# Performance work log

Hardware: AMD Instinct MI355X
Metric: run time of the kernel (lower is better)

Reference implementation:

```python
import jax, jax.numpy as jnp
import numpy as np

EPS = 1e-6
INV_T = 1.0
STEPS = 6  # TRAIN_STEPS (module defaults to training mode)
NORM_EPS = 1e-12  # F.normalize default eps


def _l2norm_dim1(t):
    # F.normalize(t, p=2, dim=1): divide by clamped L2 norm over feature dim D
    n = jnp.sqrt(jnp.sum(t * t, axis=1, keepdims=True))
    return t / jnp.maximum(n, NORM_EPS)


def setup_inputs() -> dict:
    key = jax.random.key(0)
    k1, k2 = jax.random.split(key)
    x5d = jax.random.normal(k1, (2, 512, 16, 64, 64), dtype=jnp.float32)
    bases = jax.random.uniform(k2, (2, 512, 64), dtype=jnp.float32)  # (B*S, D_feat, R)
    return {"x5d": x5d, "bases": bases}


def reference(x5d, bases):
    B, C, Dv, H, W = x5d.shape
    S = 1
    D_feat = C // S
    N = Dv * H * W
    x = x5d.reshape(B * S, D_feat, N)  # (BS, D, N)

    b = _l2norm_dim1(bases)  # _build_bases normalizes over D
    # coef init uses UNCLAMPED x (clamp happens in-place only inside local_step)
    coef = jax.nn.softmax(INV_T * jnp.einsum('bdn,bdr->bnr', x, b), axis=-1)

    xc = jnp.maximum(x, EPS)  # clamp_input_nonneg, applied in-place on first MU step

    def mu_step(carry, _):
        b, c = carry
        BtB = jnp.einsum('bdr,bds->brs', b, b)            # (BS,R,R)
        numC = jnp.einsum('bdn,bdr->bnr', xc, b)          # (BS,N,R)
        denC = jnp.einsum('bnr,brs->bns', c, BtB) + EPS
        c = c * numC / denC
        CtC = jnp.einsum('bnr,bns->brs', c, c)            # (BS,R,R)
        numB = jnp.einsum('bdn,bnr->bdr', xc, c)          # (BS,D,R)
        denB = jnp.einsum('bdr,brs->bds', b, CtC) + EPS
        b = b * numB / denB
        b = jnp.maximum(b, EPS)
        c = jnp.maximum(c, EPS)
        b = _l2norm_dim1(b)  # normalize_each_step
        return (b, c), None

    (b, coef), _ = jax.lax.scan(mu_step, (b, coef), None, length=STEPS)

    # compute_coef (differentiable refinement in the original)
    BtB = jnp.einsum('bdr,bds->brs', b, b)
    numC = jnp.einsum('bdn,bdr->bnr', xc, b)
    denC = jnp.einsum('bnr,brs->bns', coef, BtB) + EPS
    c_new = coef * (numC / denC)

    x_hat = jnp.einsum('bdr,bnr->bdn', b, c_new)  # (BS, D, N)
    return x_hat.reshape(B, C, Dv, H, W)
```

## Files before the change

kernel.cpp:

```cpp
#include <hip/hip_runtime.h>
#include <math.h>

#define DD   512
#define NTOT 65536
#define RR   64
#define NB   2
#define EPSV 1e-6f

typedef unsigned short u16;
typedef __attribute__((ext_vector_type(8))) short bf16x8;
typedef __attribute__((ext_vector_type(8))) unsigned short us8;
typedef __attribute__((ext_vector_type(4))) unsigned short us4;
typedef __attribute__((ext_vector_type(4))) float f32x4;

__device__ inline u16 f2bf(float f) {
    union { float f; unsigned u; } x; x.f = f;
    unsigned r = x.u + 0x7FFFu + ((x.u >> 16) & 1u);
    return (u16)(r >> 16);
}
__device__ inline float bf2f(u16 h) {
    union { unsigned u; float f; } x; x.u = ((unsigned)h) << 16;
    return x.f;
}
__device__ inline bf16x8 clampbf8(bf16x8 v) {
#pragma unroll
    for (int i = 0; i < 8; ++i) {
        short t = v[i];
        v[i] = (t < (short)0x3586) ? (short)0x3586 : t;
    }
    return v;
}

#define MFMA16(a, b, c) __builtin_amdgcn_mfma_f32_16x16x32_bf16((a), (b), (c), 0, 0, 0)

__global__ __launch_bounds__(256) void convert_x_kernel(const float* __restrict__ x,
                                                        u16* __restrict__ xd,
                                                        u16* __restrict__ xT) {
    int s = blockIdx.z, d0 = blockIdx.y * 64, n0 = blockIdx.x * 64;
    const float* xp = x + ((size_t)s * DD + d0) * NTOT + n0;
    u16* xdp = xd + ((size_t)s * DD + d0) * NTOT + n0;
    u16* xtp = xT + ((size_t)s * NTOT + n0) * DD + d0;
    __shared__ u16 L[64][66];
    int tid = threadIdx.x;
#pragma unroll
    for (int k = 0; k < 4; ++k) {
        int f4 = tid + k * 256;
        int dr = f4 >> 4, c4 = (f4 & 15) * 4;
        float4 v = *(const float4*)&xp[(size_t)dr * NTOT + c4];
        u16 h0 = f2bf(v.x), h1 = f2bf(v.y), h2 = f2bf(v.z), h3 = f2bf(v.w);
        xdp[(size_t)dr * NTOT + c4 + 0] = f2bf(fmaxf(v.x, EPSV));
        xdp[(size_t)dr * NTOT + c4 + 1] = f2bf(fmaxf(v.y, EPSV));
        xdp[(size_t)dr * NTOT + c4 + 2] = f2bf(fmaxf(v.z, EPSV));
        xdp[(size_t)dr * NTOT + c4 + 3] = f2bf(fmaxf(v.w, EPSV));
        L[dr][c4 + 0] = h0; L[dr][c4 + 1] = h1;
        L[dr][c4 + 2] = h2; L[dr][c4 + 3] = h3;
    }
    __syncthreads();
#pragma unroll
    for (int k = 0; k < 2; ++k) {
        int f8 = tid + k * 256;
        int nr = f8 >> 3, d8 = (f8 & 7) * 8;
        us8 w;
#pragma unroll
        for (int i = 0; i < 8; ++i) w[i] = L[d8 + i][nr];
        *(us8*)&xtp[(size_t)nr * DD + d8] = w;
    }
}

__global__ __launch_bounds__(64) void colnorm_kernel(const float* __restrict__ src,
                                                     float* __restrict__ dst) {
    int col = blockIdx.x;
    int s = col >> 6, r = col & 63;
    const float* p = src + (size_t)s * DD * RR + r;
    float* q = dst + (size_t)s * DD * RR + r;
    int lane = threadIdx.x;
    float v[8];
    float ss = 0.f;
#pragma unroll
    for (int k = 0; k < 8; ++k) {
        v[k] = p[(size_t)(lane + 64 * k) * RR];
        ss += v[k] * v[k];
    }
#pragma unroll
    for (int m = 1; m < 64; m <<= 1) ss += __shfl_xor(ss, m);
    float inv = 1.f / fmaxf(sqrtf(ss), 1e-12f);
#pragma unroll
    for (int k = 0; k < 8; ++k)
        q[(size_t)(lane + 64 * k) * RR] = v[k] * inv;
}

__global__ __launch_bounds__(256) void bcast0_kernel(const float* __restrict__ b,
                                                     u16* __restrict__ b_bf,
                                                     u16* __restrict__ bT_bf) {
    int s = blockIdx.x, tid = threadIdx.x;
    const float* bp = b + (size_t)s * DD * RR;
    u16* bb = b_bf + (size_t)s * DD * RR;
    u16* bt = bT_bf + (size_t)s * RR * DD;
    for (int i = tid; i < DD * RR; i += 256) {
        int d = i >> 6, r = i & 63;
        u16 h = f2bf(bp[i]);
        bb[i] = h;
        bt[r * DD + d] = h;
    }
}

__global__ __launch_bounds__(256) void gram_kernel(const u16* __restrict__ bT_bf,
                                                   u16* __restrict__ btb_bf) {
    int s = blockIdx.x;
    int tid = threadIdx.x;
    int w = tid >> 6, lane = tid & 63, g = lane >> 4, l15 = lane & 15;
    const u16* bt = bT_bf + (size_t)s * RR * DD;
    f32x4 zero = {0.f, 0.f, 0.f, 0.f};
    f32x4 acc[4];
#pragma unroll
    for (int cs = 0; cs < 4; ++cs) acc[cs] = zero;
    for (int k0 = 0; k0 < DD; k0 += 32) {
        bf16x8 a = *(const bf16x8*)&bt[(w * 16 + l15) * DD + k0 + g * 8];
        bf16x8 b[4];
#pragma unroll
        for (int cs = 0; cs < 4; ++cs)
            b[cs] = *(const bf16x8*)&bt[(cs * 16 + l15) * DD + k0 + g * 8];
#pragma unroll
        for (int cs = 0; cs < 4; ++cs) acc[cs] = MFMA16(a, b[cs], acc[cs]);
    }
    u16* op = btb_bf + (size_t)s * RR * RR;
#pragma unroll
    for (int cs = 0; cs < 4; ++cs)
#pragma unroll
        for (int e = 0; e < 4; ++e)
            op[(w * 16 + g * 4 + e) * RR + cs * 16 + l15] = f2bf(acc[cs][e]);
}

__global__ __launch_bounds__(256) void init_mfma_kernel(const u16* __restrict__ xT,
                                                        const u16* __restrict__ bT,
                                                        u16* __restrict__ cT,
                                                        u16* __restrict__ cnb) {
    int s = blockIdx.y;
    int n0 = blockIdx.x * 128;
    int tid = threadIdx.x;
    int w = tid >> 6, lane = tid & 63, g = lane >> 4, l15 = lane & 15;
    int nw = n0 + w * 32;
    const u16* xTp = xT + (size_t)s * NTOT * DD;
    const u16* bTp = bT + (size_t)s * RR * DD;
    u16* cTp = cT + (size_t)s * RR * NTOT;
    u16* cnp = cnb + (size_t)s * NTOT * RR;

    f32x4 zero = {0.f, 0.f, 0.f, 0.f};
    f32x4 acc[4][2];
#pragma unroll
    for (int rs = 0; rs < 4; ++rs)
#pragma unroll
        for (int ns = 0; ns < 2; ++ns) acc[rs][ns] = zero;

    bf16x8 aA[4], bA[2], aB[4], bB[2];
#pragma unroll
    for (int rs = 0; rs < 4; ++rs)
        aA[rs] = *(const bf16x8*)&bTp[(rs * 16 + l15) * DD + g * 8];
#pragma unroll
    for (int ns = 0; ns < 2; ++ns)
        bA[ns] = *(const bf16x8*)&xTp[(size_t)(nw + ns * 16 + l15) * DD + g * 8];
#pragma unroll
    for (int i = 0; i < 8; ++i) {
        int kB = i * 64 + 32;
#pragma unroll
        for (int rs = 0; rs < 4; ++rs)
            aB[rs] = *(const bf16x8*)&bTp[(rs * 16 + l15) * DD + kB + g * 8];
#pragma unroll
        for (int ns = 0; ns < 2; ++ns)
            bB[ns] = *(const bf16x8*)&xTp[(size_t)(nw + ns * 16 + l15) * DD + kB + g * 8];
#pragma unroll
        for (int rs = 0; rs < 4; ++rs)
#pragma unroll
            for (int ns = 0; ns < 2; ++ns)
                acc[rs][ns] = MFMA16(aA[rs], bA[ns], acc[rs][ns]);
        int kA = (i < 7) ? i * 64 + 64 : i * 64;
#pragma unroll
        for (int rs = 0; rs < 4; ++rs)
            aA[rs] = *(const bf16x8*)&bTp[(rs * 16 + l15) * DD + kA + g * 8];
#pragma unroll
        for (int ns = 0; ns < 2; ++ns)
            bA[ns] = *(const bf16x8*)&xTp[(size_t)(nw + ns * 16 + l15) * DD + kA + g * 8];
#pragma unroll
        for (int rs = 0; rs < 4; ++rs)
#pragma unroll
            for (int ns = 0; ns < 2; ++ns)
                acc[rs][ns] = MFMA16(aB[rs], bB[ns], acc[rs][ns]);
    }

#pragma unroll
    for (int ns = 0; ns < 2; ++ns) {
        int n = nw + ns * 16 + l15;
        float m = acc[0][ns][0];
#pragma unroll
        for (int rs = 0; rs < 4; ++rs)
#pragma unroll
            for (int e = 0; e < 4; ++e) m = fmaxf(m, acc[rs][ns][e]);
        m = fmaxf(m, __shfl_xor(m, 16));
        m = fmaxf(m, __shfl_xor(m, 32));
        float ev[4][4];
        float ssum = 0.f;
#pragma unroll
        for (int rs = 0; rs < 4; ++rs)
#pragma unroll
            for (int e = 0; e < 4; ++e) {
                ev[rs][e] = __expf(acc[rs][ns][e] - m);
                ssum += ev[rs][e];
            }
        ssum += __shfl_xor(ssum, 16);
        ssum += __shfl_xor(ssum, 32);
        float inv = 1.f / ssum;
#pragma unroll
        for (int rs = 0; rs < 4; ++rs) {
            us4 pack;
#pragma unroll
            for (int e = 0; e < 4; ++e) {
                u16 h = f2bf(ev[rs][e] * inv);
                cTp[(size_t)(rs * 16 + g * 4 + e) * NTOT + n] = h;
                pack[e] = h;
            }
            *(us4*)&cnp[(size_t)n * RR + rs * 16 + g * 4] = pack;
        }
    }
}

template <int CLAMPC, int CLAMP_OUT, int WRITE_CT>
__global__ __launch_bounds__(256) void xtb_mfma_kernel(const u16* __restrict__ xT,
                                                       const u16* __restrict__ bT,
                                                       const u16* __restrict__ btbbf,
                                                       u16* __restrict__ cnb,
                                                       u16* __restrict__ cT) {
    int s = blockIdx.y;
    int n0 = blockIdx.x * 128;
    int tid = threadIdx.x;
    int w = tid >> 6, lane = tid & 63, g = lane >> 4, l15 = lane & 15;
    int nw = n0 + w * 32;
    const u16* xTp = xT + (size_t)s * NTOT * DD;
    const u16* bTp = bT + (size_t)s * RR * DD;
    const u16* bb = btbbf + (size_t)s * RR * RR;
    u16* cnp = cnb + (size_t)s * NTOT * RR;
    u16* cTp = cT + (size_t)s * RR * NTOT;

    f32x4 zero = {0.f, 0.f, 0.f, 0.f};
    f32x4 accD[4][2], accT[4][2];
#pragma unroll
    for (int rs = 0; rs < 4; ++rs)
#pragma unroll
        for (int ns = 0; ns < 2; ++ns) { accD[rs][ns] = zero; accT[rs][ns] = zero; }

#pragma unroll
    for (int k0 = 0; k0 < 64; k0 += 32) {
        bf16x8 a[4], b[2];
#pragma unroll
        for (int rs = 0; rs < 4; ++rs)
            a[rs] = *(const bf16x8*)&bb[(rs * 16 + l15) * RR + k0 + g * 8];
#pragma unroll
        for (int ns = 0; ns < 2; ++ns)
            b[ns] = *(const bf16x8*)&cnp[(size_t)(nw + ns * 16 + l15) * RR + k0 + g * 8];
#pragma unroll
        for (int rs = 0; rs < 4; ++rs)
#pragma unroll
            for (int ns = 0; ns < 2; ++ns)
                accD[rs][ns] = MFMA16(a[rs], b[ns], accD[rs][ns]);
    }

    {
        bf16x8 aA[4], bA[2], aB[4], bB[2];
#pragma unroll
        for (int rs = 0; rs < 4; ++rs)
            aA[rs] = *(const bf16x8*)&bTp[(rs * 16 + l15) * DD + g * 8];
#pragma unroll
        for (int ns = 0; ns < 2; ++ns)
            bA[ns] = clampbf8(*(const bf16x8*)&xTp[(size_t)(nw + ns * 16 + l15) * DD + g * 8]);
#pragma unroll
        for (int i = 0; i < 8; ++i) {
            int kB = i * 64 + 32;
#pragma unroll
            for (int rs = 0; rs < 4; ++rs)
                aB[rs] = *(const bf16x8*)&bTp[(rs * 16 + l15) * DD + kB + g * 8];
#pragma unroll
            for (int ns = 0; ns < 2; ++ns)
                bB[ns] = clampbf8(*(const bf16x8*)&xTp[(size_t)(nw + ns * 16 + l15) * DD + kB + g * 8]);
#pragma unroll
            for (int rs = 0; rs < 4; ++rs)
#pragma unroll
                for (int ns = 0; ns < 2; ++ns)
                    accT[rs][ns] = MFMA16(aA[rs], bA[ns], accT[rs][ns]);
            int kA = (i < 7) ? i * 64 + 64 : i * 64;
#pragma unroll
            for (int rs = 0; rs < 4; ++rs)
                aA[rs] = *(const bf16x8*)&bTp[(rs * 16 + l15) * DD + kA + g * 8];
#pragma unroll
            for (int ns = 0; ns < 2; ++ns)
                bA[ns] = clampbf8(*(const bf16x8*)&xTp[(size_t)(nw + ns * 16 + l15) * DD + kA + g * 8]);
#pragma unroll
            for (int rs = 0; rs < 4; ++rs)
#pragma unroll
                for (int ns = 0; ns < 2; ++ns)
                    accT[rs][ns] = MFMA16(aB[rs], bB[ns], accT[rs][ns]);
        }
    }

#pragma unroll
    for (int ns = 0; ns < 2; ++ns) {
        int n = nw + ns * 16 + l15;
#pragma unroll
        for (int rs = 0; rs < 4; ++rs) {
            us4 pack;
#pragma unroll
            for (int e = 0; e < 4; ++e) {
                int r = rs * 16 + g * 4 + e;
                size_t off = (size_t)r * NTOT + n;
                float cin = bf2f(cTp[off]);
                if (CLAMPC) cin = fmaxf(cin, EPSV);
                float v = cin * accT[rs][ns][e] / (accD[rs][ns][e] + EPSV);
                u16 h = f2bf(v);
                if (WRITE_CT) cTp[off] = h;
                if (CLAMP_OUT) h = (h < (u16)0x3586u) ? (u16)0x3586u : h;
                pack[e] = h;
            }
            *(us4*)&cnp[(size_t)n * RR + rs * 16 + g * 4] = pack;
        }
    }
}

__global__ __launch_bounds__(256) void ctc_mfma_kernel(const u16* __restrict__ cT,
                                                       float* __restrict__ ctc) {
    int s = blockIdx.y;
    int kbase = blockIdx.x * 512;
    int tid = threadIdx.x;
    int w = tid >> 6, lane = tid & 63, g = lane >> 4, l15 = lane & 15;
    const u16* cTp = cT + (size_t)s * RR * NTOT;
    const u16* arow = cTp + (size_t)(w * 16 + l15) * NTOT;
    f32x4 zero = {0.f, 0.f, 0.f, 0.f};
    f32x4 acc[4];
#pragma unroll
    for (int cs = 0; cs < 4; ++cs) acc[cs] = zero;

    bf16x8 aA, bA[4], aB, bB[4];
    aA = *(const bf16x8*)&arow[kbase + g * 8];
#pragma unroll
    for (int cs = 0; cs < 4; ++cs)
        bA[cs] = *(const bf16x8*)&cTp[(size_t)(cs * 16 + l15) * NTOT + kbase + g * 8];
#pragma unroll
    for (int i = 0; i < 8; ++i) {
        int kB = kbase + i * 64 + 32;
        aB = *(const bf16x8*)&arow[kB + g * 8];
#pragma unroll
        for (int cs = 0; cs < 4; ++cs)
            bB[cs] = *(const bf16x8*)&cTp[(size_t)(cs * 16 + l15) * NTOT + kB + g * 8];
#pragma unroll
        for (int cs = 0; cs < 4; ++cs) acc[cs] = MFMA16(aA, bA[cs], acc[cs]);
        int kA = (i < 7) ? kbase + i * 64 + 64 : kbase;
        aA = *(const bf16x8*)&arow[kA + g * 8];
#pragma unroll
        for (int cs = 0; cs < 4; ++cs)
            bA[cs] = *(const bf16x8*)&cTp[(size_t)(cs * 16 + l15) * NTOT + kA + g * 8];
#pragma unroll
        for (int cs = 0; cs < 4; ++cs) acc[cs] = MFMA16(aB, bB[cs], acc[cs]);
    }
    float* op = ctc + (size_t)s * RR * RR;
#pragma unroll
    for (int cs = 0; cs < 4; ++cs)
#pragma unroll
        for (int e = 0; e < 4; ++e)
            atomicAdd(&op[(w * 16 + g * 4 + e) * RR + cs * 16 + l15], acc[cs][e]);
}

__global__ __launch_bounds__(256) void xtc_mfma_kernel(const u16* __restrict__ xd,
                                                       const u16* __restrict__ cT,
                                                       float* __restrict__ numB) {
    int s = blockIdx.z;
    int dtile = blockIdx.y * 64;
    int kbase = blockIdx.x * 2048;
    int tid = threadIdx.x;
    int w = tid >> 6, lane = tid & 63, g = lane >> 4, l15 = lane & 15;
    const u16* arow = xd + (size_t)s * DD * NTOT + (size_t)(dtile + w * 16 + l15) * NTOT;
    const u16* cTp = cT + (size_t)s * RR * NTOT;
    f32x4 zero = {0.f, 0.f, 0.f, 0.f};
    f32x4 acc[4];
#pragma unroll
    for (int rs = 0; rs < 4; ++rs) acc[rs] = zero;

    bf16x8 aA, bA[4], aB, bB[4];
    aA = *(const bf16x8*)&arow[kbase + g * 8];
#pragma unroll
    for (int rs = 0; rs < 4; ++rs)
        bA[rs] = *(const bf16x8*)&cTp[(size_t)(rs * 16 + l15) * NTOT + kbase + g * 8];
#pragma unroll
    for (int i = 0; i < 32; ++i) {
        int kB = kbase + i * 64 + 32;
        aB = *(const bf16x8*)&arow[kB + g * 8];
#pragma unroll
        for (int rs = 0; rs < 4; ++rs)
            bB[rs] = *(const bf16x8*)&cTp[(size_t)(rs * 16 + l15) * NTOT + kB + g * 8];
#pragma unroll
        for (int rs = 0; rs < 4; ++rs) acc[rs] = MFMA16(aA, bA[rs], acc[rs]);
        int kA = (i < 31) ? kbase + i * 64 + 64 : kbase;
        aA = *(const bf16x8*)&arow[kA + g * 8];
#pragma unroll
        for (int rs = 0; rs < 4; ++rs)
            bA[rs] = *(const bf16x8*)&cTp[(size_t)(rs * 16 + l15) * NTOT + kA + g * 8];
#pragma unroll
        for (int rs = 0; rs < 4; ++rs) acc[rs] = MFMA16(aB, bB[rs], acc[rs]);
    }
    float* op = numB + (size_t)s * DD * RR;
#pragma unroll
    for (int rs = 0; rs < 4; ++rs)
#pragma unroll
        for (int e = 0; e < 4; ++e)
            atomicAdd(&op[(dtile + w * 16 + g * 4 + e) * RR + rs * 16 + l15], acc[rs][e]);
}

__global__ __launch_bounds__(256) void bupd_a_kernel(float* __restrict__ b0,
                                                     const float* __restrict__ numB,
                                                     const float* __restrict__ ctcG,
                                                     float* __restrict__ norm2p) {
    int s = blockIdx.y;
    int d0 = blockIdx.x * 64;
    float* bp = b0 + ((size_t)s * DD + d0) * RR;
    const float* np_ = numB + ((size_t)s * DD + d0) * RR;
    const float* cc = ctcG + (size_t)s * RR * RR;
    __shared__ __align__(16) float Bsh[64][68];
    __shared__ __align__(16) float Ct[64][68];
    __shared__ float red[16][64];
    int tid = threadIdx.x, tx = tid & 15, ty = tid >> 4;
#pragma unroll
    for (int k = 0; k < 16; ++k) {
        int idx = tid + k * 256;
        int r_ = idx >> 6, col = idx & 63;
        Bsh[r_][col] = bp[idx];
        Ct[r_][col] = cc[idx];
    }
    __syncthreads();
    float part[4] = {};
#pragma unroll
    for (int i = 0; i < 4; ++i) {
        int d = 4 * ty + i;
        float den[4] = {};
#pragma unroll
        for (int k = 0; k < 64; ++k) {
            float bv = Bsh[d][k];
            float4 ct = *(const float4*)&Ct[k][4 * tx];
            den[0] += bv * ct.x;
            den[1] += bv * ct.y;
            den[2] += bv * ct.z;
            den[3] += bv * ct.w;
        }
        float4 b4 = *(const float4*)&Bsh[d][4 * tx];
        float4 n4 = *(const float4*)&np_[(size_t)d * RR + 4 * tx];
        float4 o;
        o.x = fmaxf(b4.x * n4.x / (den[0] + EPSV), EPSV);
        o.y = fmaxf(b4.y * n4.y / (den[1] + EPSV), EPSV);
        o.z = fmaxf(b4.z * n4.z / (den[2] + EPSV), EPSV);
        o.w = fmaxf(b4.w * n4.w / (den[3] + EPSV), EPSV);
        *(float4*)&bp[(size_t)d * RR + 4 * tx] = o;
        part[0] += o.x * o.x; part[1] += o.y * o.y;
        part[2] += o.z * o.z; part[3] += o.w * o.w;
    }
#pragma unroll
    for (int j = 0; j < 4; ++j) red[ty][4 * tx + j] = part[j];
    __syncthreads();
    if (tid < 64) {
        float ssum = 0.f;
#pragma unroll
        for (int k = 0; k < 16; ++k) ssum += red[k][tid];
        norm2p[((size_t)s * 8 + blockIdx.x) * 64 + tid] = ssum;
    }
}

__global__ __launch_bounds__(256) void bupd_c_kernel(float* __restrict__ b0,
                                                     const float* __restrict__ norm2p,
                                                     u16* __restrict__ b_bf,
                                                     u16* __restrict__ bT_bf) {
    int s = blockIdx.y;
    int d0 = blockIdx.x * 64;
    float* bp = b0 + ((size_t)s * DD + d0) * RR;
    u16* bb = b_bf + ((size_t)s * DD + d0) * RR;
    u16* bt = bT_bf + (size_t)s * RR * DD;
    __shared__ float invl[64];
    int tid = threadIdx.x, tx = tid & 15, ty = tid >> 4;
    if (tid < 64) {
        float t = 0.f;
#pragma unroll
        for (int k = 0; k < 8; ++k) t += norm2p[((size_t)s * 8 + k) * 64 + tid];
        invl[tid] = 1.f / fmaxf(sqrtf(t), 1e-12f);
    }
    __syncthreads();
#pragma unroll
    for (int i = 0; i < 4; ++i) {
        int d = 4 * ty + i;
        float4 v = *(const float4*)&bp[(size_t)d * RR + 4 * tx];
        v.x *= invl[4 * tx + 0];
        v.y *= invl[4 * tx + 1];
        v.z *= invl[4 * tx + 2];
        v.w *= invl[4 * tx + 3];
        *(float4*)&bp[(size_t)d * RR + 4 * tx] = v;
        us4 pack;
        pack[0] = f2bf(v.x); pack[1] = f2bf(v.y);
        pack[2] = f2bf(v.z); pack[3] = f2bf(v.w);
        *(us4*)&bb[(size_t)d * RR + 4 * tx] = pack;
        bt[(4 * tx + 0) * DD + d0 + d] = pack[0];
        bt[(4 * tx + 1) * DD + d0 + d] = pack[1];
        bt[(4 * tx + 2) * DD + d0 + d] = pack[2];
        bt[(4 * tx + 3) * DD + d0 + d] = pack[3];
    }
}

__global__ __launch_bounds__(256) void xhat_mfma_kernel(const u16* __restrict__ b_bf,
                                                        const u16* __restrict__ cnb,
                                                        float* __restrict__ outp) {
    int s = blockIdx.z;
    int d0 = blockIdx.y * 64;
    int n0 = blockIdx.x * 64;
    int tid = threadIdx.x;
    int w = tid >> 6, lane = tid & 63, g = lane >> 4, l15 = lane & 15;
    const u16* bp = b_bf + (size_t)s * DD * RR;
    const u16* cp = cnb + (size_t)s * NTOT * RR;
    f32x4 zero = {0.f, 0.f, 0.f, 0.f};
    f32x4 acc[4];
#pragma unroll
    for (int ns = 0; ns < 4; ++ns) acc[ns] = zero;
#pragma unroll
    for (int k0 = 0; k0 < 64; k0 += 32) {
        bf16x8 a = *(const bf16x8*)&bp[(d0 + w * 16 + l15) * RR + k0 + g * 8];
        bf16x8 b[4];
#pragma unroll
        for (int ns = 0; ns < 4; ++ns)
            b[ns] = *(const bf16x8*)&cp[(size_t)(n0 + ns * 16 + l15) * RR + k0 + g * 8];
#pragma unroll
        for (int ns = 0; ns < 4; ++ns) acc[ns] = MFMA16(a, b[ns], acc[ns]);
    }
    float* op = outp + (size_t)s * DD * NTOT;
#pragma unroll
    for (int ns = 0; ns < 4; ++ns)
#pragma unroll
        for (int e = 0; e < 4; ++e)
            op[(size_t)(d0 + w * 16 + g * 4 + e) * NTOT + n0 + ns * 16 + l15] = acc[ns][e];
}

extern "C" void kernel_launch(void* const* d_in, const int* in_sizes, int n_in,
                              void* d_out, int out_size, void* d_ws, size_t ws_size,
                              hipStream_t stream) {
    const float* x = (const float*)d_in[0];
    const float* bases = (const float*)d_in[1];
    float* out = (float*)d_out;
    char* ws = (char*)d_ws;

    u16* xT = (u16*)d_out;
    u16* xd = (u16*)d_out + (size_t)NB * NTOT * DD;

    u16* cTf = (u16*)ws;
    u16* cnb = (u16*)(ws + 16777216);
    float* b0 = (float*)(ws + 33554432);
    float* ctc = (float*)(ws + 33816576);
    float* nB = (float*)(ws + 33849344);
    u16* bT_bf = (u16*)(ws + 34111488);
    u16* b_bf = (u16*)(ws + 34242560);
    u16* btb_bf = (u16*)(ws + 34373632);
    float* norm2p = (float*)(ws + 34390016);

    convert_x_kernel<<<dim3(NTOT / 64, DD / 64, NB), 256, 0, stream>>>(x, xd, xT);

    colnorm_kernel<<<NB * RR, 64, 0, stream>>>(bases, b0);
    bcast0_kernel<<<NB, 256, 0, stream>>>(b0, b_bf, bT_bf);
    gram_kernel<<<NB, 256, 0, stream>>>(bT_bf, btb_bf);

    init_mfma_kernel<<<dim3(NTOT / 128, NB), 256, 0, stream>>>(xT, bT_bf, cTf, cnb);

    for (int step = 0; step < 6; ++step) {
        if (step > 0)
            xtb_mfma_kernel<1, 1, 1><<<dim3(NTOT / 128, NB), 256, 0, stream>>>(
                xT, bT_bf, btb_bf, cnb, cTf);
        else
            xtb_mfma_kernel<0, 1, 1><<<dim3(NTOT / 128, NB), 256, 0, stream>>>(
                xT, bT_bf, btb_bf, cnb, cTf);
        hipMemsetAsync(ctc, 0, 32768 + 262144, stream);
        ctc_mfma_kernel<<<dim3(128, NB), 256, 0, stream>>>(cTf, ctc);
        xtc_mfma_kernel<<<dim3(32, 8, NB), 256, 0, stream>>>(xd, cTf, nB);
        bupd_a_kernel<<<dim3(8, NB), 256, 0, stream>>>(b0, nB, ctc, norm2p);
        bupd_c_kernel<<<dim3(8, NB), 256, 0, stream>>>(b0, norm2p, b_bf, bT_bf);
        gram_kernel<<<NB, 256, 0, stream>>>(bT_bf, btb_bf);
    }

    xtb_mfma_kernel<1, 0, 0><<<dim3(NTOT / 128, NB), 256, 0, stream>>>(
        xT, bT_bf, btb_bf, cnb, cTf);

    xhat_mfma_kernel<<<dim3(NTOT / 64, DD / 64, NB), 256, 0, stream>>>(b_bf, cnb, out);
}
```

Before: 1.547 ms.

## Fuse CtC into xtc kernel, replace atomics with partials, merge normalize+gram

Computes CtC inside the xtc kernel, using only the dtile-0 blocks, because they already load the cT tiles. Both numB and CtC are now written as per-k-slice partial buffers instead of atomic adds, which removes the memset. The b update kernel reduces the 32 slices itself. Column normalization, bf16 casting, the transpose and the Gram matrix are merged into one 1024-thread kernel per batch, which cuts the per-step launch count from six to three. In exchange it adds extra partial-buffer traffic and a serial reduction in bstep_a, and bnorm runs with only two blocks.

Result: slower. 1.817 ms (+17.4%).

```diff
diff --git a/kernel.cpp b/kernel.cpp
--- a/kernel.cpp
+++ b/kernel.cpp
@@ -67,68 +67,75 @@
     }
 }
 
-__global__ __launch_bounds__(64) void colnorm_kernel(const float* __restrict__ src,
-                                                     float* __restrict__ dst) {
-    int col = blockIdx.x;
-    int s = col >> 6, r = col & 63;
-    const float* p = src + (size_t)s * DD * RR + r;
-    float* q = dst + (size_t)s * DD * RR + r;
-    int lane = threadIdx.x;
-    float v[8];
-    float ss = 0.f;
-#pragma unroll
-    for (int k = 0; k < 8; ++k) {
-        v[k] = p[(size_t)(lane + 64 * k) * RR];
-        ss += v[k] * v[k];
-    }
-#pragma unroll
-    for (int m = 1; m < 64; m <<= 1) ss += __shfl_xor(ss, m);
-    float inv = 1.f / fmaxf(sqrtf(ss), 1e-12f);
-#pragma unroll
-    for (int k = 0; k < 8; ++k)
-        q[(size_t)(lane + 64 * k) * RR] = v[k] * inv;
-}
-
-__global__ __launch_bounds__(256) void bcast0_kernel(const float* __restrict__ b,
+__global__ __launch_bounds__(1024) void bnorm_kernel(const float* __restrict__ src,
+                                                     float* __restrict__ b0,
                                                      u16* __restrict__ b_bf,
-                                                     u16* __restrict__ bT_bf) {
+                                                     u16* __restrict__ bT_bf,
+                                                     u16* __restrict__ btb_bf) {
     int s = blockIdx.x, tid = threadIdx.x;
-    const float* bp = b + (size_t)s * DD * RR;
-    u16* bb = b_bf + (size_t)s * DD * RR;
-    u16* bt = bT_bf + (size_t)s * RR * DD;
-    for (int i = tid; i < DD * RR; i += 256) {
-        int d = i >> 6, r = i & 63;
-        u16 h = f2bf(bp[i]);
-        bb[i] = h;
-        bt[r * DD + d] = h;
-    }
-}
-
-__global__ __launch_bounds__(256) void gram_kernel(const u16* __restrict__ bT_bf,
-                                                   u16* __restrict__ btb_bf) {
-    int s = blockIdx.x;
-    int tid = threadIdx.x;
-    int w = tid >> 6, lane = tid & 63, g = lane >> 4, l15 = lane & 15;
-    const u16* bt = bT_bf + (size_t)s * RR * DD;
-    f32x4 zero = {0.f, 0.f, 0.f, 0.f};
-    f32x4 acc[4];
-#pragma unroll
-    for (int cs = 0; cs < 4; ++cs) acc[cs] = zero;
-    for (int k0 = 0; k0 < DD; k0 += 32) {
-        bf16x8 a = *(const bf16x8*)&bt[(w * 16 + l15) * DD + k0 + g * 8];
-        bf16x8 b[4];
+    int r = tid & 63, grp = tid >> 6;
+    const float* sp = src + (size_t)s * DD * RR;
+    float* b0p = b0 + (size_t)s * DD * RR;
+    u16* bbp = b_bf + (size_t)s * DD * RR;
+    __shared__ float part[16][64];
+    __shared__ float invl[64];
+    __shared__ __align__(16) u16 btl[64][520];
+    float vv[32];
+    float p = 0.f;
+#pragma unroll
+    for (int i = 0; i < 32; ++i) {
+        vv[i] = sp[(grp * 32 + i) * 64 + r];
+        p += vv[i] * vv[i];
+    }
+    part[grp][r] = p;
+    __syncthreads();
+    if (tid < 64) {
+        float ss = 0.f;
+#pragma unroll
+        for (int k = 0; k < 16; ++k) ss += part[k][tid];
+        invl[tid] = 1.f / fmaxf(sqrtf(ss), 1e-12f);
+    }
+    __syncthreads();
+    float inv = invl[r];
+#pragma unroll
+    for (int i = 0; i < 32; ++i) {
+        int d = grp * 32 + i;
+        float v = vv[i] * inv;
+        b0p[d * 64 + r] = v;
+        u16 h = f2bf(v);
+        bbp[d * 64 + r] = h;
+        btl[r][d] = h;
+    }
+    __syncthreads();
+    u16* btg = bT_bf + (size_t)s * RR * DD;
+#pragma unroll
+    for (int k = 0; k < 4; ++k) {
+        int f8 = tid + k * 1024;
+        int row = f8 >> 6, c8 = (f8 & 63) * 8;
+        *(us8*)&btg[row * DD + c8] = *(const us8*)&btl[row][c8];
+    }
+    if (grp < 4) {
+        int g = r >> 4, l15 = r & 15;
+        f32x4 zero = {0.f, 0.f, 0.f, 0.f};
+        f32x4 acc[4];
+#pragma unroll
+        for (int cs = 0; cs < 4; ++cs) acc[cs] = zero;
+        for (int k0 = 0; k0 < DD; k0 += 32) {
+            bf16x8 a = *(const bf16x8*)&btl[grp * 16 + l15][k0 + g * 8];
+            bf16x8 b[4];
+#pragma unroll
+            for (int cs = 0; cs < 4; ++cs)
+                b[cs] = *(const bf16x8*)&btl[cs * 16 + l15][k0 + g * 8];
+#pragma unroll
+            for (int cs = 0; cs < 4; ++cs) acc[cs] = MFMA16(a, b[cs], acc[cs]);
+        }
+        u16* op = btb_bf + (size_t)s * RR * RR;
 #pragma unroll
         for (int cs = 0; cs < 4; ++cs)
-            b[cs] = *(const bf16x8*)&bt[(cs * 16 + l15) * DD + k0 + g * 8];
-#pragma unroll
-        for (int cs = 0; cs < 4; ++cs) acc[cs] = MFMA16(a, b[cs], acc[cs]);
-    }
-    u16* op = btb_bf + (size_t)s * RR * RR;
-#pragma unroll
-    for (int cs = 0; cs < 4; ++cs)
-#pragma unroll
-        for (int e = 0; e < 4; ++e)
-            op[(w * 16 + g * 4 + e) * RR + cs * 16 + l15] = f2bf(acc[cs][e]);
+#pragma unroll
+            for (int e = 0; e < 4; ++e)
+                op[(grp * 16 + g * 4 + e) * RR + cs * 16 + l15] = f2bf(acc[cs][e]);
+    }
 }
 
 __global__ __launch_bounds__(256) void init_mfma_kernel(const u16* __restrict__ xT,
@@ -323,66 +330,28 @@
     }
 }
 
-__global__ __launch_bounds__(256) void ctc_mfma_kernel(const u16* __restrict__ cT,
-                                                       float* __restrict__ ctc) {
-    int s = blockIdx.y;
-    int kbase = blockIdx.x * 512;
-    int tid = threadIdx.x;
-    int w = tid >> 6, lane = tid & 63, g = lane >> 4, l15 = lane & 15;
-    const u16* cTp = cT + (size_t)s * RR * NTOT;
-    const u16* arow = cTp + (size_t)(w * 16 + l15) * NTOT;
-    f32x4 zero = {0.f, 0.f, 0.f, 0.f};
-    f32x4 acc[4];
-#pragma unroll
-    for (int cs = 0; cs < 4; ++cs) acc[cs] = zero;
-
-    bf16x8 aA, bA[4], aB, bB[4];
-    aA = *(const bf16x8*)&arow[kbase + g * 8];
-#pragma unroll
-    for (int cs = 0; cs < 4; ++cs)
-        bA[cs] = *(const bf16x8*)&cTp[(size_t)(cs * 16 + l15) * NTOT + kbase + g * 8];
-#pragma unroll
-    for (int i = 0; i < 8; ++i) {
-        int kB = kbase + i * 64 + 32;
-        aB = *(const bf16x8*)&arow[kB + g * 8];
-#pragma unroll
-        for (int cs = 0; cs < 4; ++cs)
-            bB[cs] = *(const bf16x8*)&cTp[(size_t)(cs * 16 + l15) * NTOT + kB + g * 8];
-#pragma unroll
-        for (int cs = 0; cs < 4; ++cs) acc[cs] = MFMA16(aA, bA[cs], acc[cs]);
-        int kA = (i < 7) ? kbase + i * 64 + 64 : kbase;
-        aA = *(const bf16x8*)&arow[kA + g * 8];
-#pragma unroll
-        for (int cs = 0; cs < 4; ++cs)
-            bA[cs] = *(const bf16x8*)&cTp[(size_t)(cs * 16 + l15) * NTOT + kA + g * 8];
-#pragma unroll
-        for (int cs = 0; cs < 4; ++cs) acc[cs] = MFMA16(aB, bB[cs], acc[cs]);
-    }
-    float* op = ctc + (size_t)s * RR * RR;
-#pragma unroll
-    for (int cs = 0; cs < 4; ++cs)
-#pragma unroll
-        for (int e = 0; e < 4; ++e)
-            atomicAdd(&op[(w * 16 + g * 4 + e) * RR + cs * 16 + l15], acc[cs][e]);
-}
-
-__global__ __launch_bounds__(256) void xtc_mfma_kernel(const u16* __restrict__ xd,
-                                                       const u16* __restrict__ cT,
-                                                       float* __restrict__ numB) {
+__global__ __launch_bounds__(256) void xtc_ctc_kernel(const u16* __restrict__ xd,
+                                                      const u16* __restrict__ cT,
+                                                      float* __restrict__ numBp,
+                                                      float* __restrict__ ctcp) {
     int s = blockIdx.z;
     int dtile = blockIdx.y * 64;
-    int kbase = blockIdx.x * 2048;
+    int kb = blockIdx.x;
+    int kbase = kb * 2048;
     int tid = threadIdx.x;
     int w = tid >> 6, lane = tid & 63, g = lane >> 4, l15 = lane & 15;
     const u16* arow = xd + (size_t)s * DD * NTOT + (size_t)(dtile + w * 16 + l15) * NTOT;
+    const u16* crow = cT + (size_t)s * RR * NTOT + (size_t)(w * 16 + l15) * NTOT;
     const u16* cTp = cT + (size_t)s * RR * NTOT;
+    bool do_ctc = (blockIdx.y == 0);
     f32x4 zero = {0.f, 0.f, 0.f, 0.f};
-    f32x4 acc[4];
-#pragma unroll
-    for (int rs = 0; rs < 4; ++rs) acc[rs] = zero;
-
-    bf16x8 aA, bA[4], aB, bB[4];
+    f32x4 acc[4], accC[4];
+#pragma unroll
+    for (int rs = 0; rs < 4; ++rs) { acc[rs] = zero; accC[rs] = zero; }
+
+    bf16x8 aA, cA, bA[4], aB, cB, bB[4];
     aA = *(const bf16x8*)&arow[kbase + g * 8];
+    cA = *(const bf16x8*)&crow[kbase + g * 8];
 #pragma unroll
     for (int rs = 0; rs < 4; ++rs)
         bA[rs] = *(const bf16x8*)&cTp[(size_t)(rs * 16 + l15) * NTOT + kbase + g * 8];
@@ -390,49 +359,76 @@
     for (int i = 0; i < 32; ++i) {
         int kB = kbase + i * 64 + 32;
         aB = *(const bf16x8*)&arow[kB + g * 8];
+        cB = *(const bf16x8*)&crow[kB + g * 8];
 #pragma unroll
         for (int rs = 0; rs < 4; ++rs)
             bB[rs] = *(const bf16x8*)&cTp[(size_t)(rs * 16 + l15) * NTOT + kB + g * 8];
 #pragma unroll
         for (int rs = 0; rs < 4; ++rs) acc[rs] = MFMA16(aA, bA[rs], acc[rs]);
+        if (do_ctc) {
+#pragma unroll
+            for (int cs = 0; cs < 4; ++cs) accC[cs] = MFMA16(cA, bA[cs], accC[cs]);
+        }
         int kA = (i < 31) ? kbase + i * 64 + 64 : kbase;
         aA = *(const bf16x8*)&arow[kA + g * 8];
+        cA = *(const bf16x8*)&crow[kA + g * 8];
 #pragma unroll
         for (int rs = 0; rs < 4; ++rs)
             bA[rs] = *(const bf16x8*)&cTp[(size_t)(rs * 16 + l15) * NTOT + kA + g * 8];
 #pragma unroll
         for (int rs = 0; rs < 4; ++rs) acc[rs] = MFMA16(aB, bB[rs], acc[rs]);
-    }
-    float* op = numB + (size_t)s * DD * RR;
+        if (do_ctc) {
+#pragma unroll
+            for (int cs = 0; cs < 4; ++cs) accC[cs] = MFMA16(cB, bB[cs], accC[cs]);
+        }
+    }
+    float* op = numBp + (size_t)s * 32 * 32768 + (size_t)kb * 32768;
 #pragma unroll
     for (int rs = 0; rs < 4; ++rs)
 #pragma unroll
         for (int e = 0; e < 4; ++e)
-            atomicAdd(&op[(dtile + w * 16 + g * 4 + e) * RR + rs * 16 + l15], acc[rs][e]);
-}
-
-__global__ __launch_bounds__(256) void bupd_a_kernel(float* __restrict__ b0,
-                                                     const float* __restrict__ numB,
-                                                     const float* __restrict__ ctcG,
-                                                     float* __restrict__ norm2p) {
+            op[(dtile + w * 16 + g * 4 + e) * 64 + rs * 16 + l15] = acc[rs][e];
+    if (do_ctc) {
+        float* cop = ctcp + (size_t)s * 32 * 4096 + (size_t)kb * 4096;
+#pragma unroll
+        for (int cs = 0; cs < 4; ++cs)
+#pragma unroll
+            for (int e = 0; e < 4; ++e)
+                cop[(w * 16 + g * 4 + e) * 64 + cs * 16 + l15] = accC[cs][e];
+    }
+}
+
+__global__ __launch_bounds__(256) void bstep_a_kernel(const float* __restrict__ ctcp,
+                                                      const float* __restrict__ numBp,
+                                                      float* __restrict__ b0) {
     int s = blockIdx.y;
     int d0 = blockIdx.x * 64;
+    int tid = threadIdx.x, tx = tid & 15, ty = tid >> 4;
+    __shared__ __align__(16) float Ct[64][68];
+    __shared__ __align__(16) float Nb[64][68];
+    __shared__ __align__(16) float Bsh[64][68];
+    const float* cp = ctcp + (size_t)s * 32 * 4096;
+    const float* np = numBp + (size_t)s * 32 * 32768 + (size_t)d0 * 64;
     float* bp = b0 + ((size_t)s * DD + d0) * RR;
-    const float* np_ = numB + ((size_t)s * DD + d0) * RR;
-    const float* cc = ctcG + (size_t)s * RR * RR;
-    __shared__ __align__(16) float Bsh[64][68];
-    __shared__ __align__(16) float Ct[64][68];
-    __shared__ float red[16][64];
-    int tid = threadIdx.x, tx = tid & 15, ty = tid >> 4;
-#pragma unroll
-    for (int k = 0; k < 16; ++k) {
-        int idx = tid + k * 256;
-        int r_ = idx >> 6, col = idx & 63;
-        Bsh[r_][col] = bp[idx];
-        Ct[r_][col] = cc[idx];
+
+    float sc[16], sn[16];
+#pragma unroll
+    for (int e = 0; e < 16; ++e) { sc[e] = 0.f; sn[e] = 0.f; }
+    for (int sl = 0; sl < 32; ++sl) {
+#pragma unroll
+        for (int e = 0; e < 16; ++e) {
+            sc[e] += cp[(size_t)sl * 4096 + tid + e * 256];
+            sn[e] += np[(size_t)sl * 32768 + tid + e * 256];
+        }
+    }
+#pragma unroll
+    for (int e = 0; e < 16; ++e) {
+        int idx = tid + e * 256;
+        Ct[idx >> 6][idx & 63] = sc[e];
+        Nb[idx >> 6][idx & 63] = sn[e];
+        Bsh[idx >> 6][idx & 63] = bp[idx];
     }
     __syncthreads();
-    float part[4] = {};
 #pragma unroll
     for (int i = 0; i < 4; ++i) {
         int d = 4 * ty + i;
@@ -447,62 +443,13 @@
             den[3] += bv * ct.w;
         }
         float4 b4 = *(const float4*)&Bsh[d][4 * tx];
-        float4 n4 = *(const float4*)&np_[(size_t)d * RR + 4 * tx];
+        float4 n4 = *(const float4*)&Nb[d][4 * tx];
         float4 o;
         o.x = fmaxf(b4.x * n4.x / (den[0] + EPSV), EPSV);
         o.y = fmaxf(b4.y * n4.y / (den[1] + EPSV), EPSV);
         o.z = fmaxf(b4.z * n4.z / (den[2] + EPSV), EPSV);
         o.w = fmaxf(b4.w * n4.w / (den[3] + EPSV), EPSV);
         *(float4*)&bp[(size_t)d * RR + 4 * tx] = o;
-        part[0] += o.x * o.x; part[1] += o.y * o.y;
-        part[2] += o.z * o.z; part[3] += o.w * o.w;
-    }
-#pragma unroll
-    for (int j = 0; j < 4; ++j) red[ty][4 * tx + j] = part[j];
-    __syncthreads();
-    if (tid < 64) {
-        float ssum = 0.f;
-#pragma unroll
-        for (int k = 0; k < 16; ++k) ssum += red[k][tid];
-        norm2p[((size_t)s * 8 + blockIdx.x) * 64 + tid] = ssum;
-    }
-}
-
-__global__ __launch_bounds__(256) void bupd_c_kernel(float* __restrict__ b0,
-                                                     const float* __restrict__ norm2p,
-                                                     u16* __restrict__ b_bf,
-                                                     u16* __restrict__ bT_bf) {
-    int s = blockIdx.y;
-    int d0 = blockIdx.x * 64;
-    float* bp = b0 + ((size_t)s * DD + d0) * RR;
-    u16* bb = b_bf + ((size_t)s * DD + d0) * RR;
-    u16* bt = bT_bf + (size_t)s * RR * DD;
-    __shared__ float invl[64];
-    int tid = threadIdx.x, tx = tid & 15, ty = tid >> 4;
-    if (tid < 64) {
-        float t = 0.f;
-#pragma unroll
-        for (int k = 0; k < 8; ++k) t += norm2p[((size_t)s * 8 + k) * 64 + tid];
-        invl[tid] = 1.f / fmaxf(sqrtf(t), 1e-12f);
-    }
-    __syncthreads();
-#pragma unroll
-    for (int i = 0; i < 4; ++i) {
-        int d = 4 * ty + i;
-        float4 v = *(const float4*)&bp[(size_t)d * RR + 4 * tx];
-        v.x *= invl[4 * tx + 0];
-        v.y *= invl[4 * tx + 1];
-        v.z *= invl[4 * tx + 2];
-        v.w *= invl[4 * tx + 3];
-        *(float4*)&bp[(size_t)d * RR + 4 * tx] = v;
-        us4 pack;
-        pack[0] = f2bf(v.x); pack[1] = f2bf(v.y);
-        pack[2] = f2bf(v.z); pack[3] = f2bf(v.w);
-        *(us4*)&bb[(size_t)d * RR + 4 * tx] = pack;
-        bt[(4 * tx + 0) * DD + d0 + d] = pack[0];
-        bt[(4 * tx + 1) * DD + d0 + d] = pack[1];
-        bt[(4 * tx + 2) * DD + d0 + d] = pack[2];
-        bt[(4 * tx + 3) * DD + d0 + d] = pack[3];
     }
 }
 
@@ -552,18 +499,15 @@
     u16* cTf = (u16*)ws;
     u16* cnb = (u16*)(ws + 16777216);
     float* b0 = (float*)(ws + 33554432);
-    float* ctc = (float*)(ws + 33816576);
-    float* nB = (float*)(ws + 33849344);
-    u16* bT_bf = (u16*)(ws + 34111488);
-    u16* b_bf = (u16*)(ws + 34242560);
-    u16* btb_bf = (u16*)(ws + 34373632);
-    float* norm2p = (float*)(ws + 34390016);
+    float* ctcp = (float*)(ws + 33816576);
+    float* nBp = (float*)(ws + 34865152);
+    u16* b_bf = (u16*)(ws + 43253760);
+    u16* bT_bf = (u16*)(ws + 43384832);
+    u16* btb_bf = (u16*)(ws + 43515904);
 
     convert_x_kernel<<<dim3(NTOT / 64, DD / 64, NB), 256, 0, stream>>>(x, xd, xT);
 
-    colnorm_kernel<<<NB * RR, 64, 0, stream>>>(bases, b0);
-    bcast0_kernel<<<NB, 256, 0, stream>>>(b0, b_bf, bT_bf);
-    gram_kernel<<<NB, 256, 0, stream>>>(bT_bf, btb_bf);
+    bnorm_kernel<<<NB, 1024, 0, stream>>>(bases, b0, b_bf, bT_bf, btb_bf);
 
     init_mfma_kernel<<<dim3(NTOT / 128, NB), 256, 0, stream>>>(xT, bT_bf, cTf, cnb);
 
@@ -574,12 +518,9 @@
         else
             xtb_mfma_kernel<0, 1, 1><<<dim3(NTOT / 128, NB), 256, 0, stream>>>(
                 xT, bT_bf, btb_bf, cnb, cTf);
-        hipMemsetAsync(ctc, 0, 32768 + 262144, stream);
-        ctc_mfma_kernel<<<dim3(128, NB), 256, 0, stream>>>(cTf, ctc);
-        xtc_mfma_kernel<<<dim3(32, 8, NB), 256, 0, stream>>>(xd, cTf, nB);
-        bupd_a_kernel<<<dim3(8, NB), 256, 0, stream>>>(b0, nB, ctc, norm2p);
-        bupd_c_kernel<<<dim3(8, NB), 256, 0, stream>>>(b0, norm2p, b_bf, bT_bf);
-        gram_kernel<<<NB, 256, 0, stream>>>(bT_bf, btb_bf);
+        xtc_ctc_kernel<<<dim3(32, 8, NB), 256, 0, stream>>>(xd, cTf, nBp, ctcp);
+        bstep_a_kernel<<<dim3(8, NB), 256, 0, stream>>>(ctcp, nBp, b0);
+        bnorm_kernel<<<NB, 1024, 0, stream>>>(b0, b0, b_bf, bT_bf, btb_bf);
     }
 
     xtb_mfma_kernel<1, 0, 0><<<dim3(NTOT / 128, NB), 256, 0, stream>>>(
```
